# Kernel tuning notes

Hardware: AMD Instinct MI355X
Metric: run time of the kernel (lower is better)

Reference implementation:

```python
import jax, jax.numpy as jnp
import numpy as np

NEG = -1000000.0

def setup_inputs() -> dict:
    key = jax.random.key(0)
    k1, k2, k3, k4, k5 = jax.random.split(key, 5)
    B, Lq, Lm, Din, Dout = 8, 2048, 2048, 1024, 1024
    query = jax.random.normal(k1, (B, Lq, Din), dtype=jnp.float32)
    memories = jax.random.normal(k2, (B, Lm, Dout), dtype=jnp.float32)
    mask = jax.random.randint(k3, (B, Lq, Lm), 0, 2, dtype=jnp.int32)
    # Linear(in_features=1024, out_features=1024)
    bound = 1.0 / np.sqrt(Din)
    W = jax.random.uniform(k4, (Dout, Din), minval=-bound, maxval=bound, dtype=jnp.float32)
    b = jax.random.uniform(k5, (Dout,), minval=-bound, maxval=bound, dtype=jnp.float32)
    return {"query": query, "memories": memories, "mask": mask, "W": W, "b": b}

def reference(query, memories, mask, W, b):
    # projected query: [B, Lq, Dout]
    q = jnp.einsum('bqi,oi->bqo', query, W) + b
    # additive binary mask: 1 -> 0, 0 -> -1e6
    add_mask = (1.0 - mask.astype(q.dtype)) * NEG
    # unscaled Luong scores: [B, Lq, Lm]
    logits = jnp.einsum('bqd,bmd->bqm', q, memories) + add_mask
    weights = jax.nn.softmax(logits, axis=-1)
    out = jnp.einsum('bqm,bmd->bqd', weights, memories)
    return out
```

## Files before the change

### kernel.cpp

```cpp
#include <hip/hip_runtime.h>

typedef float    f32x4 __attribute__((ext_vector_type(4)));
typedef _Float16 f16x4 __attribute__((ext_vector_type(4)));
typedef _Float16 f16x8 __attribute__((ext_vector_type(8)));

__device__ __forceinline__ void gload16(const void* g, void* l) {
  __builtin_amdgcn_global_load_lds(
      (const __attribute__((address_space(1))) void*)g,
      (__attribute__((address_space(3))) void*)l, 16, 0, 0);
}

#define MFMA16(d, a, b) __builtin_amdgcn_mfma_f32_16x16x32_f16(a, b, d, 0, 0, 0)

template <bool STG>
__device__ __forceinline__ void ktile256(
    char* L, int d, size_t go,
    const char* aSrc0, const char* aSrc1,
    const char* bSrc0, const char* bSrc1,
    int ldsStage, int wr, int wc, int l15, int rcb,
    f32x4 (&acc)[8][4]) {
  const char* Ab0 = L + d * 32768;
  const char* Bb0 = L + 65536 + d * 32768;
  const int dn = d ^ 1;

  if constexpr (STG) {
    char* dA = L + dn * 32768 + ldsStage;
    char* dB = L + 65536 + dn * 32768 + ldsStage;
    gload16(aSrc0 + go, dA);
    gload16(aSrc1 + go, dA + 1024);
    gload16(aSrc0 + go + 64, dA + 16384);
    gload16(aSrc1 + go + 64, dA + 16384 + 1024);
    gload16(bSrc0 + go, dB);
    gload16(bSrc1 + go, dB + 1024);
    gload16(bSrc0 + go + 64, dB + 16384);
    gload16(bSrc1 + go + 64, dB + 16384 + 1024);
  }

  f16x8 afX[4], afY[4], bfX[4], bfY[4];

  #pragma unroll
  for (int m = 0; m < 4; m++)
    afX[m] = *(const f16x8*)(Ab0 + (wr + m * 16 + l15) * 64 + rcb);
  #pragma unroll
  for (int n = 0; n < 4; n++)
    bfX[n] = *(const f16x8*)(Bb0 + (wc + n * 16 + l15) * 64 + rcb);
  #pragma unroll
  for (int m = 0; m < 4; m++)
    afY[m] = *(const f16x8*)(Ab0 + (wr + (4 + m) * 16 + l15) * 64 + rcb);

  __builtin_amdgcn_s_setprio(1);
  #pragma unroll
  for (int m = 0; m < 4; m++)
    #pragma unroll
    for (int n = 0; n < 4; n++)
      acc[m][n] = MFMA16(acc[m][n], afX[m], bfX[n]);
  __builtin_amdgcn_s_setprio(0);

  #pragma unroll
  for (int n = 0; n < 4; n++)
    bfY[n] = *(const f16x8*)(Bb0 + 16384 + (wc + n * 16 + l15) * 64 + rcb);
  #pragma unroll
  for (int m = 0; m < 4; m++)
    afX[m] = *(const f16x8*)(Ab0 + 16384 + (wr + m * 16 + l15) * 64 + rcb);

  __builtin_amdgcn_s_setprio(1);
  #pragma unroll
  for (int m = 0; m < 4; m++)
    #pragma unroll
    for (int n = 0; n < 4; n++)
      acc[4 + m][n] = MFMA16(acc[4 + m][n], afY[m], bfX[n]);
  __builtin_amdgcn_s_setprio(0);

  #pragma unroll
  for (int m = 0; m < 4; m++)
    afY[m] = *(const f16x8*)(Ab0 + 16384 + (wr + (4 + m) * 16 + l15) * 64 + rcb);

  __builtin_amdgcn_s_setprio(1);
  #pragma unroll
  for (int m = 0; m < 4; m++)
    #pragma unroll
    for (int n = 0; n < 4; n++)
      acc[m][n] = MFMA16(acc[m][n], afX[m], bfY[n]);
  __builtin_amdgcn_s_setprio(0);

  __builtin_amdgcn_s_setprio(1);
  #pragma unroll
  for (int m = 0; m < 4; m++)
    #pragma unroll
    for (int n = 0; n < 4; n++)
      acc[4 + m][n] = MFMA16(acc[4 + m][n], afY[m], bfY[n]);
  __builtin_amdgcn_s_setprio(0);

  if constexpr (STG) {
    asm volatile("s_waitcnt vmcnt(0)" ::: "memory");
    __builtin_amdgcn_s_barrier();
  }
}

template <typename TOUT, bool BIAS>
__global__ __launch_bounds__(512) void gemm256(
    const _Float16* __restrict__ A, const _Float16* __restrict__ B,
    const float* __restrict__ bias, TOUT* __restrict__ Cp,
    int M, int N, int K, long sA, long sB, long sC) {
  __shared__ _Float16 lds[65536];
  char* const L = (char*)lds;
  const int tid = threadIdx.x;
  const int w = tid >> 6, l = tid & 63;
  const int l15 = l & 15, q = l >> 4;
  const int wr = (w >> 2) * 128, wc = (w & 3) * 64;

  const int gx = gridDim.x, gy = gridDim.y;
  const int nwg = gx * gy * gridDim.z;
  const int lin = (blockIdx.z * gy + blockIdx.y) * gx + blockIdx.x;
  const int li = (lin & 7) * (nwg >> 3) + (lin >> 3);
  const int bx = li % gx;
  const int t1 = li / gx;
  const int by = t1 % gy;
  const int bz = t1 / gy;

  const int m0 = by * 256, n0 = bx * 256;
  const _Float16* Ab = A + (size_t)bz * sA;
  const _Float16* Bb = B + (size_t)bz * sB;

  const int scb = (((l & 3) ^ ((l >> 3) & 3)) << 4);
  const int sr0 = w * 32 + (l >> 2);
  const char* aSrc0 = (const char*)(Ab + (size_t)(m0 + sr0) * K) + scb;
  const char* aSrc1 = (const char*)(Ab + (size_t)(m0 + sr0 + 16) * K) + scb;
  const char* bSrc0 = (const char*)(Bb + (size_t)(n0 + sr0) * K) + scb;
  const char* bSrc1 = (const char*)(Bb + (size_t)(n0 + sr0 + 16) * K) + scb;
  const int ldsStage = w * 2048;
  const int rcb = ((q ^ ((l15 >> 1) & 3)) << 4);

  f32x4 acc[8][4] = {};
  const int NT = K >> 6;

  {
    char* dA = L + ldsStage;
    char* dB = L + 65536 + ldsStage;
    gload16(aSrc0, dA);       gload16(aSrc1, dA + 1024);
    gload16(aSrc0 + 64, dA + 16384); gload16(aSrc1 + 64, dA + 16384 + 1024);
    gload16(bSrc0, dB);       gload16(bSrc1, dB + 1024);
    gload16(bSrc0 + 64, dB + 16384); gload16(bSrc1 + 64, dB + 16384 + 1024);
    asm volatile("s_waitcnt vmcnt(0)" ::: "memory");
  }
  __builtin_amdgcn_s_barrier();

  for (int t = 0; t < NT - 1; ++t)
    ktile256<true>(L, t & 1, (size_t)(t + 1) * 128, aSrc0, aSrc1, bSrc0, bSrc1,
                   ldsStage, wr, wc, l15, rcb, acc);
  ktile256<false>(L, (NT - 1) & 1, 0, aSrc0, aSrc1, bSrc0, bSrc1,
                  ldsStage, wr, wc, l15, rcb, acc);

  TOUT* C = Cp + (size_t)bz * sC;
  const int q4 = q * 4;
  #pragma unroll
  for (int n = 0; n < 4; n++) {
    int col = n0 + wc + n * 16 + l15;
    float bb = BIAS ? bias[col] : 0.0f;
    #pragma unroll
    for (int m = 0; m < 8; m++) {
      int rowb = m0 + wr + m * 16 + q4;
      #pragma unroll
      for (int rr = 0; rr < 4; rr++)
        C[(size_t)(rowb + rr) * N + col] = (TOUT)(acc[m][n][rr] + bb);
    }
  }
}

__global__ __launch_bounds__(256) void transpose16_kernel(
    const _Float16* __restrict__ src, _Float16* __restrict__ dst) {
  const int Lm = 2048, D = 1024;
  __shared__ _Float16 tile[64 * 64];
  const int d0 = blockIdx.x * 64, m0 = blockIdx.y * 64;
  const _Float16* s = src + (size_t)blockIdx.z * Lm * D;
  _Float16*       d = dst + (size_t)blockIdx.z * D * Lm;
  const int tid = threadIdx.x;
  #pragma unroll
  for (int it = 0; it < 2; it++) {
    int idx = tid + it * 256;
    int mm = idx >> 3, g = idx & 7;
    int pg = g ^ ((mm >> 3) & 7);
    *(f16x8*)&tile[mm * 64 + pg * 8] =
        *(const f16x8*)&s[(size_t)(m0 + mm) * D + d0 + g * 8];
  }
  __syncthreads();
  #pragma unroll
  for (int it = 0; it < 2; it++) {
    int idx = tid + it * 256;
    int dd = idx >> 3, mc = (idx & 7) * 8;
    f16x8 h;
    #pragma unroll
    for (int j = 0; j < 8; j++) {
      int row = mc + j;
      int pg = (dd >> 3) ^ ((row >> 3) & 7);
      h[j] = tile[row * 64 + pg * 8 + (dd & 7)];
    }
    *(f16x8*)&d[(size_t)(d0 + dd) * Lm + m0 + mc] = h;
  }
}

__global__ __launch_bounds__(256) void softmax_kernel(
    const int* __restrict__ mask, _Float16* __restrict__ wbuf) {
  const int Lm = 2048;
  size_t row = blockIdx.x;
  _Float16* wr = wbuf + row * Lm;
  const int* mr = mask + row * Lm;
  int tid = threadIdx.x;
  f16x8 lv = *(const f16x8*)&wr[tid * 8];
  int4 ma = *(const int4*)&mr[tid * 8];
  int4 mb = *(const int4*)&mr[tid * 8 + 4];
  int mk[8] = {ma.x, ma.y, ma.z, ma.w, mb.x, mb.y, mb.z, mb.w};
  float v[8];
  float mx = -3.0e38f;
  #pragma unroll
  for (int i = 0; i < 8; i++) {
    float l = (float)lv[i];
    if (mk[i] == 0) l += -1000000.0f;
    v[i] = l;
    mx = fmaxf(mx, l);
  }
  #pragma unroll
  for (int off = 32; off > 0; off >>= 1) mx = fmaxf(mx, __shfl_down(mx, off, 64));
  __shared__ float red[4];
  int wv = tid >> 6;
  if ((tid & 63) == 0) red[wv] = mx;
  __syncthreads();
  mx = fmaxf(fmaxf(red[0], red[1]), fmaxf(red[2], red[3]));
  __syncthreads();
  float s = 0.f;
  #pragma unroll
  for (int i = 0; i < 8; i++) { v[i] = __expf(v[i] - mx); s += v[i]; }
  #pragma unroll
  for (int off = 32; off > 0; off >>= 1) s += __shfl_down(s, off, 64);
  if ((tid & 63) == 0) red[wv] = s;
  __syncthreads();
  float inv = 1.0f / (red[0] + red[1] + red[2] + red[3]);
  f16x8 o;
  #pragma unroll
  for (int i = 0; i < 8; i++) o[i] = (_Float16)(v[i] * inv);
  *(f16x8*)&wr[tid * 8] = o;
}

__global__ __launch_bounds__(256) void cvt8_kernel(const float* __restrict__ x,
                                                   _Float16* __restrict__ y) {
  size_t i = (size_t)(blockIdx.x * 256 + threadIdx.x) * 8;
  f32x4 a = *(const f32x4*)&x[i];
  f32x4 b = *(const f32x4*)&x[i + 4];
  f16x8 h = {(_Float16)a[0], (_Float16)a[1], (_Float16)a[2], (_Float16)a[3],
             (_Float16)b[0], (_Float16)b[1], (_Float16)b[2], (_Float16)b[3]};
  *(f16x8*)&y[i] = h;
}

extern "C" void kernel_launch(void* const* d_in, const int* in_sizes, int n_in,
                              void* d_out, int out_size, void* d_ws, size_t ws_size,
                              hipStream_t stream) {
  const float* query = (const float*)d_in[0];
  const float* mem   = (const float*)d_in[1];
  const int*   mask  = (const int*)d_in[2];
  const float* W     = (const float*)d_in[3];
  const float* bias  = (const float*)d_in[4];
  float* out = (float*)d_out;

  char* ws = (char*)d_ws;
  _Float16* qproj  = (_Float16*)ws;
  _Float16* memT   = (_Float16*)ws;
  _Float16* queryh = (_Float16*)(ws + (size_t)32 * 1024 * 1024);
  _Float16* Wh     = (_Float16*)(ws + (size_t)64 * 1024 * 1024);
  _Float16* wbuf   = (_Float16*)(ws + (size_t)32 * 1024 * 1024);
  _Float16* memh   = (_Float16*)d_out;

  const long LQK = 2048L * 1024, LQM = 2048L * 2048;

  cvt8_kernel<<<dim3(512),  256, 0, stream>>>(W, Wh);
  cvt8_kernel<<<dim3(8192), 256, 0, stream>>>(query, queryh);
  cvt8_kernel<<<dim3(8192), 256, 0, stream>>>(mem, memh);
  gemm256<_Float16, true><<<dim3(4, 64, 1), 512, 0, stream>>>(
      queryh, Wh, bias, qproj, 16384, 1024, 1024, 0, 0, 0);
  gemm256<_Float16, false><<<dim3(8, 8, 8), 512, 0, stream>>>(
      qproj, memh, nullptr, wbuf, 2048, 2048, 1024, LQK, LQK, LQM);
  softmax_kernel<<<dim3(16384), 256, 0, stream>>>(mask, wbuf);
  transpose16_kernel<<<dim3(16, 32, 8), 256, 0, stream>>>(memh, memT);
  gemm256<float, false><<<dim3(4, 8, 8), 512, 0, stream>>>(
      wbuf, memT, nullptr, out, 2048, 1024, 2048, LQM, LQK, LQK);
}
```

Baseline: 489.1 us.

## Restructure GEMM main loop into fine-grained staged pipeline and fuse mask into epilogue

Rewrites the 256x256 GEMM K-loop into four sub-phases. Each phase issues a slice of the next tile's global-to-LDS loads, uses partial vmcnt waits and barriers, and runs MFMAs on the previous tile's second half. The aim is to interleave memory traffic with compute more evenly instead of loading the whole tile up front and waiting at the end. It also moves mask application into the logits GEMM epilogue, writing -60000 for masked entries, so the softmax kernel no longer reads the int mask. The cost is many more barriers and an epilogue that reads the mask with strided access.

```diff
diff --git a/kernel.cpp b/kernel.cpp
--- a/kernel.cpp
+++ b/kernel.cpp
@@ -11,97 +11,25 @@
 }
 
 #define MFMA16(d, a, b) __builtin_amdgcn_mfma_f32_16x16x32_f16(a, b, d, 0, 0, 0)
-
-template <bool STG>
-__device__ __forceinline__ void ktile256(
-    char* L, int d, size_t go,
-    const char* aSrc0, const char* aSrc1,
-    const char* bSrc0, const char* bSrc1,
-    int ldsStage, int wr, int wc, int l15, int rcb,
-    f32x4 (&acc)[8][4]) {
-  const char* Ab0 = L + d * 32768;
-  const char* Bb0 = L + 65536 + d * 32768;
-  const int dn = d ^ 1;
-
-  if constexpr (STG) {
-    char* dA = L + dn * 32768 + ldsStage;
-    char* dB = L + 65536 + dn * 32768 + ldsStage;
-    gload16(aSrc0 + go, dA);
-    gload16(aSrc1 + go, dA + 1024);
-    gload16(aSrc0 + go + 64, dA + 16384);
-    gload16(aSrc1 + go + 64, dA + 16384 + 1024);
-    gload16(bSrc0 + go, dB);
-    gload16(bSrc1 + go, dB + 1024);
-    gload16(bSrc0 + go + 64, dB + 16384);
-    gload16(bSrc1 + go + 64, dB + 16384 + 1024);
-  }
-
-  f16x8 afX[4], afY[4], bfX[4], bfY[4];
-
-  #pragma unroll
-  for (int m = 0; m < 4; m++)
-    afX[m] = *(const f16x8*)(Ab0 + (wr + m * 16 + l15) * 64 + rcb);
-  #pragma unroll
-  for (int n = 0; n < 4; n++)
-    bfX[n] = *(const f16x8*)(Bb0 + (wc + n * 16 + l15) * 64 + rcb);
-  #pragma unroll
-  for (int m = 0; m < 4; m++)
-    afY[m] = *(const f16x8*)(Ab0 + (wr + (4 + m) * 16 + l15) * 64 + rcb);
-
-  __builtin_amdgcn_s_setprio(1);
-  #pragma unroll
-  for (int m = 0; m < 4; m++)
-    #pragma unroll
-    for (int n = 0; n < 4; n++)
-      acc[m][n] = MFMA16(acc[m][n], afX[m], bfX[n]);
-  __builtin_amdgcn_s_setprio(0);
-
-  #pragma unroll
-  for (int n = 0; n < 4; n++)
-    bfY[n] = *(const f16x8*)(Bb0 + 16384 + (wc + n * 16 + l15) * 64 + rcb);
-  #pragma unroll
-  for (int m = 0; m < 4; m++)
-    afX[m] = *(const f16x8*)(Ab0 + 16384 + (wr + m * 16 + l15) * 64 + rcb);
-
-  __builtin_amdgcn_s_setprio(1);
-  #pragma unroll
-  for (int m = 0; m < 4; m++)
-    #pragma unroll
-    for (int n = 0; n < 4; n++)
-      acc[4 + m][n] = MFMA16(acc[4 + m][n], afY[m], bfX[n]);
-  __builtin_amdgcn_s_setprio(0);
-
-  #pragma unroll
-  for (int m = 0; m < 4; m++)
-    afY[m] = *(const f16x8*)(Ab0 + 16384 + (wr + (4 + m) * 16 + l15) * 64 + rcb);
-
-  __builtin_amdgcn_s_setprio(1);
-  #pragma unroll
-  for (int m = 0; m < 4; m++)
-    #pragma unroll
-    for (int n = 0; n < 4; n++)
-      acc[m][n] = MFMA16(acc[m][n], afX[m], bfY[n]);
-  __builtin_amdgcn_s_setprio(0);
-
-  __builtin_amdgcn_s_setprio(1);
-  #pragma unroll
-  for (int m = 0; m < 4; m++)
-    #pragma unroll
-    for (int n = 0; n < 4; n++)
-      acc[4 + m][n] = MFMA16(acc[4 + m][n], afY[m], bfY[n]);
-  __builtin_amdgcn_s_setprio(0);
-
-  if constexpr (STG) {
-    asm volatile("s_waitcnt vmcnt(0)" ::: "memory");
-    __builtin_amdgcn_s_barrier();
-  }
-}
-
-template <typename TOUT, bool BIAS>
+#define VMCNT(n) asm volatile("s_waitcnt vmcnt(" #n ")" ::: "memory")
+#define LGKM0()  asm volatile("s_waitcnt lgkmcnt(0)" ::: "memory")
+#define SB0()    __builtin_amdgcn_sched_barrier(0)
+#define BAR()    __builtin_amdgcn_s_barrier()
+
+#define G_LO(af, bf)                                  \
+  _Pragma("unroll") for (int m_ = 0; m_ < 4; m_++)    \
+  _Pragma("unroll") for (int n_ = 0; n_ < 4; n_++)    \
+      acc[m_][n_] = MFMA16(acc[m_][n_], af[m_], bf[n_]);
+#define G_HI(af, bf)                                  \
+  _Pragma("unroll") for (int m_ = 0; m_ < 4; m_++)    \
+  _Pragma("unroll") for (int n_ = 0; n_ < 4; n_++)    \
+      acc[4 + m_][n_] = MFMA16(acc[4 + m_][n_], af[m_], bf[n_]);
+
+template <typename TOUT, bool BIAS, bool MASK>
 __global__ __launch_bounds__(512) void gemm256(
     const _Float16* __restrict__ A, const _Float16* __restrict__ B,
-    const float* __restrict__ bias, TOUT* __restrict__ Cp,
-    int M, int N, int K, long sA, long sB, long sC) {
+    const float* __restrict__ bias, const int* __restrict__ mask,
+    TOUT* __restrict__ Cp, int M, int N, int K, long sA, long sB, long sC) {
   __shared__ _Float16 lds[65536];
   char* const L = (char*)lds;
   const int tid = threadIdx.x;
@@ -123,35 +51,116 @@
   const _Float16* Bb = B + (size_t)bz * sB;
 
   const int scb = (((l & 3) ^ ((l >> 3) & 3)) << 4);
-  const int sr0 = w * 32 + (l >> 2);
-  const char* aSrc0 = (const char*)(Ab + (size_t)(m0 + sr0) * K) + scb;
-  const char* aSrc1 = (const char*)(Ab + (size_t)(m0 + sr0 + 16) * K) + scb;
-  const char* bSrc0 = (const char*)(Bb + (size_t)(n0 + sr0) * K) + scb;
-  const char* bSrc1 = (const char*)(Bb + (size_t)(n0 + sr0 + 16) * K) + scb;
-  const int ldsStage = w * 2048;
+  const int sr = w * 16 + (l >> 2);
+  const long rowB = (long)K * 2;
+  const char* aS  = (const char*)Ab + (size_t)(m0 + sr) * rowB + scb;
+  const char* aS2 = aS + 128 * rowB;
+  const char* bS  = (const char*)Bb + (size_t)(n0 + sr) * rowB + scb;
+  const char* bS2 = bS + 128 * rowB;
+  const int stW = w * 1024;
   const int rcb = ((q ^ ((l15 >> 1) & 3)) << 4);
+  const int aOff = (wr + l15) * 64 + rcb;
+  const int bOff = 65536 + (wc + l15) * 64 + rcb;
 
   f32x4 acc[8][4] = {};
   const int NT = K >> 6;
 
+  gload16(bS, L + 65536 + stW);              gload16(bS2, L + 65536 + stW + 8192);
+  gload16(aS, L + stW);                      gload16(aS2, L + stW + 8192);
+  gload16(aS + 64, L + 16384 + stW);         gload16(aS2 + 64, L + 16384 + stW + 8192);
+  gload16(bS + 64, L + 65536 + 16384 + stW); gload16(bS2 + 64, L + 65536 + 16384 + stW + 8192);
+
+  f16x8 af[4], bf[4];
+
+  for (int t = 0; t < NT - 1; ++t) {
+    const int d = t & 1, dn = d ^ 1, tn = t + 1;
+    const char* pAo = L + aOff + dn * 32768;
+    const char* pBo = L + bOff + dn * 32768;
+    const char* pAc = L + aOff + d * 32768;
+    const char* pBc = L + bOff + d * 32768;
+    char* const sbA = L + dn * 32768 + stW;
+    const int go = tn * 128;
+
+    if (t) {
+      #pragma unroll
+      for (int m = 0; m < 4; m++) af[m] = *(const f16x8*)(pAo + 16384 + m * 1024);
+      #pragma unroll
+      for (int n = 0; n < 4; n++) bf[n] = *(const f16x8*)(pBo + 16384 + n * 1024);
+    }
+    gload16(bS + go, sbA + 65536); gload16(bS2 + go, sbA + 65536 + 8192);
+    VMCNT(6); BAR(); LGKM0(); SB0();
+    if (t) { __builtin_amdgcn_s_setprio(1); G_LO(af, bf); __builtin_amdgcn_s_setprio(0); }
+    BAR(); SB0();
+
+    if (t) {
+      #pragma unroll
+      for (int m = 0; m < 4; m++) af[m] = *(const f16x8*)(pAo + 16384 + 4096 + m * 1024);
+    }
+    gload16(aS + go, sbA); gload16(aS2 + go, sbA + 8192);
+    VMCNT(6); BAR(); LGKM0(); SB0();
+    if (t) { __builtin_amdgcn_s_setprio(1); G_HI(af, bf); __builtin_amdgcn_s_setprio(0); }
+    BAR(); SB0();
+
+    #pragma unroll
+    for (int m = 0; m < 4; m++) af[m] = *(const f16x8*)(pAc + m * 1024);
+    #pragma unroll
+    for (int n = 0; n < 4; n++) bf[n] = *(const f16x8*)(pBc + n * 1024);
+    gload16(aS + go + 64, sbA + 16384); gload16(aS2 + go + 64, sbA + 16384 + 8192);
+    VMCNT(6); BAR(); LGKM0(); SB0();
+    __builtin_amdgcn_s_setprio(1); G_LO(af, bf); __builtin_amdgcn_s_setprio(0);
+    BAR(); SB0();
+
+    #pragma unroll
+    for (int m = 0; m < 4; m++) af[m] = *(const f16x8*)(pAc + 4096 + m * 1024);
+    gload16(bS + go + 64, sbA + 65536 + 16384); gload16(bS2 + go + 64, sbA + 65536 + 16384 + 8192);
+    VMCNT(6); BAR(); LGKM0(); SB0();
+    __builtin_amdgcn_s_setprio(1); G_HI(af, bf); __builtin_amdgcn_s_setprio(0);
+    BAR(); SB0();
+  }
+
   {
-    char* dA = L + ldsStage;
-    char* dB = L + 65536 + ldsStage;
-    gload16(aSrc0, dA);       gload16(aSrc1, dA + 1024);
-    gload16(aSrc0 + 64, dA + 16384); gload16(aSrc1 + 64, dA + 16384 + 1024);
-    gload16(bSrc0, dB);       gload16(bSrc1, dB + 1024);
-    gload16(bSrc0 + 64, dB + 16384); gload16(bSrc1 + 64, dB + 16384 + 1024);
-    asm volatile("s_waitcnt vmcnt(0)" ::: "memory");
-  }
-  __builtin_amdgcn_s_barrier();
-
-  for (int t = 0; t < NT - 1; ++t)
-    ktile256<true>(L, t & 1, (size_t)(t + 1) * 128, aSrc0, aSrc1, bSrc0, bSrc1,
-                   ldsStage, wr, wc, l15, rcb, acc);
-  ktile256<false>(L, (NT - 1) & 1, 0, aSrc0, aSrc1, bSrc0, bSrc1,
-                  ldsStage, wr, wc, l15, rcb, acc);
+    const int d = (NT - 1) & 1, dn = d ^ 1;
+    const char* pAo = L + aOff + dn * 32768;
+    const char* pBo = L + bOff + dn * 32768;
+    const char* pAc = L + aOff + d * 32768;
+    const char* pBc = L + bOff + d * 32768;
+
+    #pragma unroll
+    for (int m = 0; m < 4; m++) af[m] = *(const f16x8*)(pAo + 16384 + m * 1024);
+    #pragma unroll
+    for (int n = 0; n < 4; n++) bf[n] = *(const f16x8*)(pBo + 16384 + n * 1024);
+    BAR(); LGKM0(); SB0();
+    __builtin_amdgcn_s_setprio(1); G_LO(af, bf); __builtin_amdgcn_s_setprio(0);
+    BAR(); SB0();
+    #pragma unroll
+    for (int m = 0; m < 4; m++) af[m] = *(const f16x8*)(pAo + 16384 + 4096 + m * 1024);
+    VMCNT(4); BAR(); LGKM0(); SB0();
+    __builtin_amdgcn_s_setprio(1); G_HI(af, bf); __builtin_amdgcn_s_setprio(0);
+    BAR(); SB0();
+    #pragma unroll
+    for (int m = 0; m < 4; m++) af[m] = *(const f16x8*)(pAc + m * 1024);
+    #pragma unroll
+    for (int n = 0; n < 4; n++) bf[n] = *(const f16x8*)(pBc + n * 1024);
+    BAR(); LGKM0(); SB0();
+    __builtin_amdgcn_s_setprio(1); G_LO(af, bf); __builtin_amdgcn_s_setprio(0);
+    BAR(); SB0();
+    #pragma unroll
+    for (int m = 0; m < 4; m++) af[m] = *(const f16x8*)(pAc + 4096 + m * 1024);
+    VMCNT(0); BAR(); LGKM0(); SB0();
+    __builtin_amdgcn_s_setprio(1); G_HI(af, bf); __builtin_amdgcn_s_setprio(0);
+    BAR(); SB0();
+    #pragma unroll
+    for (int m = 0; m < 4; m++) af[m] = *(const f16x8*)(pAc + 16384 + m * 1024);
+    #pragma unroll
+    for (int n = 0; n < 4; n++) bf[n] = *(const f16x8*)(pBc + 16384 + n * 1024);
+    G_LO(af, bf);
+    #pragma unroll
+    for (int m = 0; m < 4; m++) af[m] = *(const f16x8*)(pAc + 16384 + 4096 + m * 1024);
+    G_HI(af, bf);
+  }
 
   TOUT* C = Cp + (size_t)bz * sC;
+  const int* Mb = MASK ? (mask + (size_t)bz * ((size_t)M * N)) : nullptr;
   const int q4 = q * 4;
   #pragma unroll
   for (int n = 0; n < 4; n++) {
@@ -161,8 +170,12 @@
     for (int m = 0; m < 8; m++) {
       int rowb = m0 + wr + m * 16 + q4;
       #pragma unroll
-      for (int rr = 0; rr < 4; rr++)
-        C[(size_t)(rowb + rr) * N + col] = (TOUT)(acc[m][n][rr] + bb);
+      for (int rr = 0; rr < 4; rr++) {
+        float v = acc[m][n][rr] + bb;
+        if constexpr (MASK)
+          if (Mb[(size_t)(rowb + rr) * N + col] == 0) v = -60000.0f;
+        C[(size_t)(rowb + rr) * N + col] = (TOUT)v;
+      }
     }
   }
 }
@@ -199,25 +212,18 @@
   }
 }
 
-__global__ __launch_bounds__(256) void softmax_kernel(
-    const int* __restrict__ mask, _Float16* __restrict__ wbuf) {
+__global__ __launch_bounds__(256) void softmax_kernel(_Float16* __restrict__ wbuf) {
   const int Lm = 2048;
   size_t row = blockIdx.x;
   _Float16* wr = wbuf + row * Lm;
-  const int* mr = mask + row * Lm;
   int tid = threadIdx.x;
   f16x8 lv = *(const f16x8*)&wr[tid * 8];
-  int4 ma = *(const int4*)&mr[tid * 8];
-  int4 mb = *(const int4*)&mr[tid * 8 + 4];
-  int mk[8] = {ma.x, ma.y, ma.z, ma.w, mb.x, mb.y, mb.z, mb.w};
   float v[8];
   float mx = -3.0e38f;
   #pragma unroll
   for (int i = 0; i < 8; i++) {
-    float l = (float)lv[i];
-    if (mk[i] == 0) l += -1000000.0f;
-    v[i] = l;
-    mx = fmaxf(mx, l);
+    v[i] = (float)lv[i];
+    mx = fmaxf(mx, v[i]);
   }
   #pragma unroll
   for (int off = 32; off > 0; off >>= 1) mx = fmaxf(mx, __shfl_down(mx, off, 64));
@@ -274,12 +280,12 @@
   cvt8_kernel<<<dim3(512),  256, 0, stream>>>(W, Wh);
   cvt8_kernel<<<dim3(8192), 256, 0, stream>>>(query, queryh);
   cvt8_kernel<<<dim3(8192), 256, 0, stream>>>(mem, memh);
-  gemm256<_Float16, true><<<dim3(4, 64, 1), 512, 0, stream>>>(
-      queryh, Wh, bias, qproj, 16384, 1024, 1024, 0, 0, 0);
-  gemm256<_Float16, false><<<dim3(8, 8, 8), 512, 0, stream>>>(
-      qproj, memh, nullptr, wbuf, 2048, 2048, 1024, LQK, LQK, LQM);
-  softmax_kernel<<<dim3(16384), 256, 0, stream>>>(mask, wbuf);
+  gemm256<_Float16, true, false><<<dim3(4, 64, 1), 512, 0, stream>>>(
+      queryh, Wh, bias, nullptr, qproj, 16384, 1024, 1024, 0, 0, 0);
+  gemm256<_Float16, false, true><<<dim3(8, 8, 8), 512, 0, stream>>>(
+      qproj, memh, nullptr, mask, wbuf, 2048, 2048, 1024, LQK, LQK, LQM);
+  softmax_kernel<<<dim3(16384), 256, 0, stream>>>(wbuf);
   transpose16_kernel<<<dim3(16, 32, 8), 256, 0, stream>>>(memh, memT);
-  gemm256<float, false><<<dim3(4, 8, 8), 512, 0, stream>>>(
-      wbuf, memT, nullptr, out, 2048, 1024, 2048, LQM, LQK, LQK);
-}
+  gemm256<float, false, false><<<dim3(4, 8, 8), 512, 0, stream>>>(
+      wbuf, memT, nullptr, nullptr, out, 2048, 1024, 2048, LQM, LQK, LQK);
+}
```

New measurement: 580.1 us. +18.6%, slower.
